# Kernel tuning notes

Hardware: AMD Instinct MI355X
Metric: run time of the kernel (lower is better)

Reference implementation:

```python
import jax, jax.numpy as jnp
import numpy as np

B, S, D, H = 2, 2048, 768, 12
HD = D // H  # head_dim = 64


def setup_inputs() -> dict:
    key = jax.random.key(0)
    ks = jax.random.split(key, 9)
    s = 1.0 / np.sqrt(D)
    return {
        "x": jax.random.normal(ks[0], (B, S, D), dtype=jnp.float32),
        "Wq": jax.random.normal(ks[1], (D, D), dtype=jnp.float32) * s,
        "bq": jnp.zeros((D,), dtype=jnp.float32),
        "Wk": jax.random.normal(ks[2], (D, D), dtype=jnp.float32) * s,
        "bk": jnp.zeros((D,), dtype=jnp.float32),
        "Wv": jax.random.normal(ks[3], (D, D), dtype=jnp.float32) * s,
        "bv": jnp.zeros((D,), dtype=jnp.float32),
        "Wo": jax.random.normal(ks[4], (D, D), dtype=jnp.float32) * s,
        "bo": jnpp if False else jnp.zeros((D,), dtype=jnp.float32),
    }


def reference(x, Wq, bq, Wk, bk, Wv, bv, Wo, bo):
    b, s, d = x.shape
    # projections, split heads: [b, h, s, hd]
    def proj(W, bias):
        y = x @ W + bias
        return y.reshape(b, s, H, HD).transpose(0, 2, 1, 3)

    q = proj(Wq, bq)
    k = proj(Wk, bk)
    v = proj(Wv, bv)

    scale = 1.0 / jnp.sqrt(jnp.float32(HD))
    scores = jnp.einsum("bhqd,bhkd->bhqk", q, k) * scale
    causal = jnp.tril(jnp.ones((s, s), dtype=bool))  # True where allowed
    scores = jnp.where(causal, scores, -jnp.inf)
    attn = jax.nn.softmax(scores, axis=-1)
    ctx = jnp.einsum("bhqk,bhkd->bhqd", attn, v)
    ctx = ctx.transpose(0, 2, 1, 3).reshape(b, s, d)
    return ctx @ Wo + bo
```

## Files before the change

### kernel.cpp

```cpp
#include <hip/hip_runtime.h>
#include <stdint.h>

typedef unsigned short u16;
typedef __attribute__((ext_vector_type(8))) short s16x8;
typedef __attribute__((ext_vector_type(4))) float f32x4;
typedef __attribute__((ext_vector_type(16))) float f32x16;

#define MFMA_BF16(a, b, c) __builtin_amdgcn_mfma_f32_16x16x32_bf16((a), (b), (c), 0, 0, 0)
#define MFMA32(a, b, c) __builtin_amdgcn_mfma_f32_32x32x16_bf16((a), (b), (c), 0, 0, 0)

typedef const __attribute__((address_space(1))) uint32_t* gas1_t;
typedef __attribute__((address_space(3))) uint32_t* las3_t;
#define GLDS16(dst, src) __builtin_amdgcn_global_load_lds((gas1_t)(src), (las3_t)(dst), 16, 0, 0)

static __device__ __forceinline__ u16 f2bf(float f) {
    uint32_t u = __float_as_uint(f);
    u = (u + 0x7fffu + ((u >> 16) & 1u)) >> 16;
    return (u16)u;
}
static __device__ __forceinline__ uint32_t pk2bf(float a, float b) {
    return (uint32_t)f2bf(a) | ((uint32_t)f2bf(b) << 16);
}
static __device__ __forceinline__ float bf2f(u16 h) {
    return __uint_as_float(((uint32_t)h) << 16);
}

__global__ __launch_bounds__(256) void k_prep(const float* __restrict__ x, u16* __restrict__ xb,
                                              const float* __restrict__ w0, const float* __restrict__ w1,
                                              const float* __restrict__ w2, const float* __restrict__ w3,
                                              u16* __restrict__ t0, u16* __restrict__ t1,
                                              u16* __restrict__ t2, u16* __restrict__ t3) {
    __shared__ float tile[32][33];
    const int bid = blockIdx.x, t = threadIdx.x;
    if (bid < 1536) {
        const int i = (bid * 256 + t) * 8;
        f32x4 a = *(const f32x4*)(x + i);
        f32x4 b = *(const f32x4*)(x + i + 4);
        s16x8 r;
        r[0] = (short)f2bf(a[0]); r[1] = (short)f2bf(a[1]);
        r[2] = (short)f2bf(a[2]); r[3] = (short)f2bf(a[3]);
        r[4] = (short)f2bf(b[0]); r[5] = (short)f2bf(b[1]);
        r[6] = (short)f2bf(b[2]); r[7] = (short)f2bf(b[3]);
        *(s16x8*)(xb + i) = r;
        return;
    }
    const int u = bid - 1536;
    const int z = u / 576, r2 = u - z * 576;
    const float* W; u16* T;
    switch (z) {
        case 0:  W = w0; T = t0; break;
        case 1:  W = w1; T = t1; break;
        case 2:  W = w2; T = t2; break;
        default: W = w3; T = t3; break;
    }
    const int n0 = (r2 % 24) * 32, k0 = (r2 / 24) * 32;
    const int tx = t & 31, ty = t >> 5;
#pragma unroll
    for (int i = 0; i < 4; ++i)
        tile[ty + 8 * i][tx] = W[(size_t)(k0 + ty + 8 * i) * 768 + n0 + tx];
    __syncthreads();
#pragma unroll
    for (int i = 0; i < 4; ++i)
        T[(size_t)(n0 + ty + 8 * i) * 768 + k0 + tx] = f2bf(tile[tx][ty + 8 * i]);
}

__global__ __launch_bounds__(256) void k_gemm_qkv(
        const u16* __restrict__ A,
        const u16* __restrict__ btq, const u16* __restrict__ btk, const u16* __restrict__ btv,
        const float* __restrict__ bq, const float* __restrict__ bk, const float* __restrict__ bv,
        u16* __restrict__ outq, u16* __restrict__ outk, u16* __restrict__ outv) {
    __shared__ u16 lA[128 * 64];
    __shared__ u16 lB[64 * 64];
    const int cid = blockIdx.x;
    const int swz = (cid & 7) * 144 + (cid >> 3);
    const int sx = swz % 36, by = swz / 36;
    const int sel = sx / 12, nb = sx - sel * 12;
    const u16* Bt; const float* bias;
    if (sel == 0)      { Bt = btq; bias = bq; }
    else if (sel == 1) { Bt = btk; bias = bk; }
    else               { Bt = btv; bias = bv; }
    const int t = threadIdx.x, lane = t & 63, w = t >> 6;
    const int wr = w >> 1, wc = w & 1;
    const int c = lane & 15, g = lane >> 4;
    const int m0 = by * 128, n0 = nb * 64;
    f32x4 acc[4][2] = {};
    const int lr = lane >> 3, lg = lane & 7;
    const int swz8 = 8 * (lg ^ lr);
    const u16* gA = A  + (size_t)(m0 + w * 8 + lr) * 768 + swz8;
    const u16* gB = Bt + (size_t)(n0 + w * 8 + lr) * 768 + swz8;
    for (int kb = 0; kb < 768; kb += 64) {
#pragma unroll
        for (int j = 0; j < 4; ++j)
            GLDS16(&lA[j * 2048 + w * 512], gA + (size_t)j * 32 * 768 + kb);
#pragma unroll
        for (int j = 0; j < 2; ++j)
            GLDS16(&lB[j * 2048 + w * 512], gB + (size_t)j * 32 * 768 + kb);
        __syncthreads();
#pragma unroll
        for (int kh = 0; kh < 2; ++kh) {
            s16x8 af[4], bfr[2];
            const int gg = kh * 4 + g;
#pragma unroll
            for (int i = 0; i < 4; ++i) {
                const int ra = wr * 64 + i * 16 + c;
                af[i] = *(const s16x8*)&lA[ra * 64 + 8 * (gg ^ (ra & 7))];
            }
#pragma unroll
            for (int j = 0; j < 2; ++j) {
                const int rb = wc * 32 + j * 16 + c;
                bfr[j] = *(const s16x8*)&lB[rb * 64 + 8 * (gg ^ (rb & 7))];
            }
#pragma unroll
            for (int i = 0; i < 4; ++i)
#pragma unroll
                for (int j = 0; j < 2; ++j)
                    acc[i][j] = MFMA_BF16(af[i], bfr[j], acc[i][j]);
        }
        __syncthreads();
    }
    const float C2 = 0.18033688011112042f;
    const int h = nb;
    if (sel < 2) {
        u16* outp = (sel == 0) ? outq : outk;
        const float osc = (sel == 0) ? C2 : 1.0f;
#pragma unroll
        for (int i = 0; i < 4; ++i)
#pragma unroll
            for (int j = 0; j < 2; ++j) {
                const int hd = wc * 32 + j * 16 + c;
                const float bvv = bias[n0 + hd];
#pragma unroll
                for (int rr = 0; rr < 4; ++rr) {
                    const int m = m0 + wr * 64 + i * 16 + g * 4 + rr;
                    const int b = m >> 11, s = m & 2047;
                    outp[(((size_t)(b * 12 + h) * 2048 + s) << 6) + hd] =
                        f2bf((acc[i][j][rr] + bvv) * osc);
                }
            }
    } else {
#pragma unroll
        for (int i = 0; i < 4; ++i)
#pragma unroll
            for (int j = 0; j < 2; ++j) {
                const int hd = wc * 32 + j * 16 + c;
                const float bvv = bias[n0 + hd];
                const int m = m0 + wr * 64 + i * 16 + g * 4;
                const int b = m >> 11, s = m & 2047;
                uint64_t pk = (uint64_t)pk2bf(acc[i][j][0] + bvv, acc[i][j][1] + bvv) |
                              ((uint64_t)pk2bf(acc[i][j][2] + bvv, acc[i][j][3] + bvv) << 32);
                *(uint64_t*)&outv[((size_t)(b * 12 + h) * 64 + hd) * 2048 + s] = pk;
            }
    }
}

__global__ __launch_bounds__(256) void k_gemm_out(const u16* __restrict__ A,
                                                  const u16* __restrict__ Bt,
                                                  const float* __restrict__ bias,
                                                  float* __restrict__ out) {
    __shared__ u16 lA[64 * 64];
    __shared__ u16 lB[64 * 64];
    const int cid = blockIdx.x;
    const int swz = (cid & 7) * 96 + (cid >> 3);
    const int bx = swz % 12, by = swz / 12;
    const int t = threadIdx.x;
    const int lane = t & 63, w = t >> 6;
    const int wr = w >> 1, wc = w & 1;
    const int c = lane & 15, g = lane >> 4;
    const int m0 = by * 64, n0 = bx * 64;
    f32x4 acc[2][2] = {};
    const int lr = lane >> 3, lq = lane & 7;
    const int sq = (lq ^ lr) * 8;
    const u16* gA0 = A  + (size_t)(m0 + w * 16 + lr) * 768 + sq;
    const u16* gA1 = gA0 + 8 * 768;
    const u16* gB0 = Bt + (size_t)(n0 + w * 16 + lr) * 768 + sq;
    const u16* gB1 = gB0 + 8 * 768;
    u16* dA0 = &lA[w * 1024];
    u16* dA1 = &lA[w * 1024 + 512];
    u16* dB0 = &lB[w * 1024];
    u16* dB1 = &lB[w * 1024 + 512];
    for (int kb = 0; kb < 768; kb += 64) {
        GLDS16(dA0, gA0 + kb); GLDS16(dA1, gA1 + kb);
        GLDS16(dB0, gB0 + kb); GLDS16(dB1, gB1 + kb);
        __syncthreads();
#pragma unroll
        for (int st = 0; st < 2; ++st) {
            s16x8 af[2], bf[2];
            const int col = st * 32 + g * 8;
#pragma unroll
            for (int i = 0; i < 2; ++i) {
                int ra = wr * 32 + i * 16 + c;
                af[i] = *(const s16x8*)&lA[ra * 64 + (col ^ ((ra & 7) << 3))];
                int rb = wc * 32 + i * 16 + c;
                bf[i] = *(const s16x8*)&lB[rb * 64 + (col ^ ((rb & 7) << 3))];
            }
#pragma unroll
            for (int i = 0; i < 2; ++i)
#pragma unroll
                for (int j = 0; j < 2; ++j)
                    acc[i][j] = MFMA_BF16(af[i], bf[j], acc[i][j]);
        }
        __syncthreads();
    }
#pragma unroll
    for (int i = 0; i < 2; ++i)
#pragma unroll
        for (int j = 0; j < 2; ++j) {
            const int n = n0 + wc * 32 + j * 16 + c;
            const float bvv = bias[n];
#pragma unroll
            for (int rr = 0; rr < 4; ++rr) {
                const int m = m0 + wr * 32 + i * 16 + g * 4 + rr;
                out[(size_t)m * 768 + n] = acc[i][j][rr] + bvv;
            }
        }
}

__device__ static const signed char SLOT_QT[40] = {
    15,15,15,15, 14,14,14,14, 13,13,13,13, 12,12,12,12,
    11,11,11, 10,10,10, 9,9,9, 8,8,8, 7,7, 6,6, 5,5, 4,4, 3, 2, 1, 0};
__device__ static const signed char SLOT_SEG[40] = {
    0,1,2,3, 0,1,2,3, 0,1,2,3, 0,1,2,3,
    0,1,2, 0,1,2, 0,1,2, 0,1,2, 0,1, 0,1, 0,1, 0,1, 0, 0, 0, 0};

__global__ __launch_bounds__(256) void k_attn(const u16* __restrict__ qw,
                                              const u16* __restrict__ kw,
                                              const u16* __restrict__ vt,
                                              u16* __restrict__ ctxb,
                                              u16* __restrict__ pctx,
                                              float* __restrict__ pm,
                                              float* __restrict__ ps) {
    __shared__ u16 lK[2][64 * 64];
    __shared__ u16 lV[2][64 * 64];
    const int bid = blockIdx.x;
    const int slot = bid / 24, j24 = bid - slot * 24;
    const int bh = (j24 & 7) * 3 + (j24 >> 3);
    const int qt = SLOT_QT[slot], seg = SLOT_SEG[slot];
    const int nseg = (2 * (qt + 1) + 7) >> 3;
    const int ch0 = seg * 8;
    const int rem = 2 * (qt + 1) - ch0;
    const int nch = rem < 8 ? rem : 8;
    const int t = threadIdx.x, lane = t & 63, w = t >> 6;
    const int l31 = lane & 31, hi = lane >> 5;
    const int q0w = qt * 128 + w * 32;
    const u16* qp = qw + (size_t)bh * 2048 * 64;
    const u16* kp = kw + (size_t)bh * 2048 * 64;
    const u16* vp = vt + (size_t)bh * 64 * 2048;
    s16x8 qf[4];
#pragma unroll
    for (int dk = 0; dk < 4; ++dk)
        qf[dk] = *(const s16x8*)&qp[(size_t)(q0w + l31) * 64 + dk * 16 + hi * 8];
    asm volatile("s_waitcnt vmcnt(0)" ::: "memory");
    const int lr = lane >> 3, lg = lane & 7;
    const int swz8 = 8 * (lg ^ lr);
    const u16* kpb = kp + (size_t)(w * 16 + lr) * 64 + swz8;
    const u16* vpb = vp + (size_t)(w * 16 + lr) * 2048 + swz8;
    const int lastq = q0w + 31;
    f32x16 ct[2] = {};
    float m2 = -1e30f, ssum = 0.0f;
#define STAGE(bf, ch)                                                          \
    {                                                                          \
        const u16* ks_ = kpb + (size_t)(ch) * 4096;                            \
        GLDS16(&lK[bf][(w * 16) * 64], ks_);                                   \
        GLDS16(&lK[bf][(w * 16 + 8) * 64], ks_ + 8 * 64);                      \
        const u16* vs_ = vpb + (size_t)(ch) * 64;                              \
        GLDS16(&lV[bf][(w * 16) * 64], vs_);                                   \
        GLDS16(&lV[bf][(w * 16 + 8) * 64], vs_ + 8 * 2048);                    \
    }
    STAGE(0, ch0);
    for (int ci = 0; ci < nch; ++ci) {
        const int bf = ci & 1, Kc = (ch0 + ci) * 64;
        if (ci + 1 < nch) {
            STAGE(bf ^ 1, ch0 + ci + 1);
            asm volatile("s_waitcnt vmcnt(4)" ::: "memory");
        } else {
            asm volatile("s_waitcnt vmcnt(0)" ::: "memory");
        }
        __builtin_amdgcn_sched_barrier(0);
        __builtin_amdgcn_s_barrier();
        if (Kc <= lastq) {
            f32x16 st[2] = {};
            __builtin_amdgcn_s_setprio(1);
#pragma unroll
            for (int dk = 0; dk < 4; ++dk) {
                const int gr = dk * 2 + hi;
                const int r0 = l31, r1 = 32 + l31;
                s16x8 kf0 = *(const s16x8*)&lK[bf][r0 * 64 + 8 * (gr ^ (r0 & 7))];
                s16x8 kf1 = *(const s16x8*)&lK[bf][r1 * 64 + 8 * (gr ^ (r1 & 7))];
                st[0] = MFMA32(kf0, qf[dk], st[0]);
                st[1] = MFMA32(kf1, qf[dk], st[1]);
            }
            __builtin_amdgcn_s_setprio(0);
            const int qg = q0w + l31;
            float tv[32];
            if (Kc + 63 <= q0w) {
#pragma unroll
                for (int j = 0; j < 16; ++j) { tv[j] = st[0][j]; tv[16 + j] = st[1][j]; }
            } else {
                const int kb = Kc + 4 * hi;
#pragma unroll
                for (int j = 0; j < 16; ++j) {
                    const int kloc = (j & 3) + 8 * (j >> 2);
                    tv[j]      = (kb + kloc      <= qg) ? st[0][j] : -1e30f;
                    tv[16 + j] = (kb + kloc + 32 <= qg) ? st[1][j] : -1e30f;
                }
            }
            float x16[16], x8[8], x4[4];
#pragma unroll
            for (int j = 0; j < 16; ++j) x16[j] = fmaxf(tv[j], tv[j + 16]);
#pragma unroll
            for (int j = 0; j < 8; ++j) x8[j] = fmaxf(x16[j], x16[j + 8]);
#pragma unroll
            for (int j = 0; j < 4; ++j) x4[j] = fmaxf(x8[j], x8[j + 4]);
            const float mt = fmaxf(fmaxf(x4[0], x4[1]), fmaxf(x4[2], x4[3]));
            if (!__all(mt <= m2 + 8.0f)) {
                float mq = fmaxf(mt, __shfl_xor(mt, 32));
                const float mnew = fmaxf(m2, mq);
                const float fac = __builtin_amdgcn_exp2f(m2 - mnew);
                ssum *= fac;
#pragma unroll
                for (int j = 0; j < 16; ++j) { ct[0][j] *= fac; ct[1][j] *= fac; }
                m2 = mnew;
            }
            float p[32];
#pragma unroll
            for (int j = 0; j < 32; ++j) p[j] = __builtin_amdgcn_exp2f(tv[j] - m2);
            float y16[16], y8[8], y4[4];
#pragma unroll
            for (int j = 0; j < 16; ++j) y16[j] = p[j] + p[j + 16];
#pragma unroll
            for (int j = 0; j < 8; ++j) y8[j] = y16[j] + y16[j + 8];
#pragma unroll
            for (int j = 0; j < 4; ++j) y4[j] = y8[j] + y8[j + 4];
            ssum += (y4[0] + y4[1]) + (y4[2] + y4[3]);
#pragma unroll
            for (int kt = 0; kt < 2; ++kt) {
                uint32_t pcv[8];
#pragma unroll
                for (int x = 0; x < 8; ++x) {
                    const int j = kt * 16 + 4 * (x >> 1) + 2 * (x & 1);
                    asm volatile("v_cvt_pk_bf16_f32 %0, %1, %2"
                                 : "=v"(pcv[x]) : "v"(p[j]), "v"(p[j + 1]));
                }
#pragma unroll
                for (int kl = 0; kl < 2; ++kl) {
                    uint32_t a0 = pcv[4 * kl],     b0 = pcv[4 * kl + 2];
                    uint32_t a1 = pcv[4 * kl + 1], b1 = pcv[4 * kl + 3];
                    asm volatile("v_permlane32_swap_b32 %0, %1" : "+v"(a0), "+v"(b0));
                    asm volatile("v_permlane32_swap_b32 %0, %1" : "+v"(a1), "+v"(b1));
                    union { uint32_t u[4]; s16x8 v; } pf;
                    pf.u[0] = a0; pf.u[1] = a1; pf.u[2] = b0; pf.u[3] = b1;
                    const int gr = (kt * 2 + kl) * 2 + hi;
                    const int rv0 = l31, rv1 = 32 + l31;
                    s16x8 vf0 = *(const s16x8*)&lV[bf][rv0 * 64 + 8 * (gr ^ (rv0 & 7))];
                    s16x8 vf1 = *(const s16x8*)&lV[bf][rv1 * 64 + 8 * (gr ^ (rv1 & 7))];
                    __builtin_amdgcn_s_setprio(1);
                    ct[0] = MFMA32(vf0, pf.v, ct[0]);
                    ct[1] = MFMA32(vf1, pf.v, ct[1]);
                    __builtin_amdgcn_s_setprio(0);
                }
            }
        }
        __builtin_amdgcn_s_barrier();
    }
    if (nseg == 1) {
        ssum += __shfl_xor(ssum, 32);
        const float inv = 1.0f / ssum;
        const int b = bh / 12, h = bh - b * 12;
        const size_t base = (size_t)(b * 2048 + q0w + l31) * 768 + h * 64;
#pragma unroll
        for (int ht = 0; ht < 2; ++ht)
#pragma unroll
            for (int a = 0; a < 4; ++a) {
                const int hd = ht * 32 + 8 * a + 4 * hi;
                uint64_t pk = (uint64_t)pk2bf(ct[ht][4 * a] * inv, ct[ht][4 * a + 1] * inv) |
                              ((uint64_t)pk2bf(ct[ht][4 * a + 2] * inv, ct[ht][4 * a + 3] * inv) << 32);
                *(uint64_t*)&ctxb[base + hd] = pk;
            }
    } else {
        const float srow = ssum + __shfl_xor(ssum, 32);
        const int ti = (bh * 16 + qt) * 4 + seg;
        const int row = w * 32 + l31;
        u16* pp = &pctx[(size_t)ti * 8192 + row * 64];
#pragma unroll
        for (int ht = 0; ht < 2; ++ht)
#pragma unroll
            for (int a = 0; a < 4; ++a) {
                const int hd = ht * 32 + 8 * a + 4 * hi;
                uint64_t pk = (uint64_t)pk2bf(ct[ht][4 * a], ct[ht][4 * a + 1]) |
                              ((uint64_t)pk2bf(ct[ht][4 * a + 2], ct[ht][4 * a + 3]) << 32);
                *(uint64_t*)&pp[hd] = pk;
            }
        if (hi == 0) {
            pm[ti * 128 + row] = m2;
            ps[ti * 128 + row] = srow;
        }
    }
#undef STAGE
}

__global__ __launch_bounds__(256) void k_attn_combine(const u16* __restrict__ pctx,
                                                      const float* __restrict__ pm,
                                                      const float* __restrict__ ps,
                                                      u16* __restrict__ ctxb) {
    const int bh = blockIdx.x, qt = blockIdx.y + 4;
    const int nseg = (2 * (qt + 1) + 7) >> 3;
    const int tb = (bh * 16 + qt) * 4;
    const int b = bh / 12, h = bh - b * 12;
#pragma unroll
    for (int it = 0; it < 2; ++it) {
        const int u = threadIdx.x + it * 256;
        const int row = u >> 2, h0 = (u & 3) * 16;
        float mv[4], sv[4];
#pragma unroll
        for (int s = 0; s < 4; ++s) {
            mv[s] = (s < nseg) ? pm[(tb + s) * 128 + row] : -1e30f;
            sv[s] = (s < nseg) ? ps[(tb + s) * 128 + row] : 0.0f;
        }
        const float mstar = fmaxf(fmaxf(mv[0], mv[1]), fmaxf(mv[2], mv[3]));
        float wv[4], S = 0.0f;
#pragma unroll
        for (int s = 0; s < 4; ++s) {
            wv[s] = __builtin_amdgcn_exp2f(mv[s] - mstar);
            S += wv[s] * sv[s];
        }
        float acc[16] = {};
#pragma unroll
        for (int s = 0; s < 4; ++s) {
            if (s < nseg) {
                const u16* pp = &pctx[(size_t)(tb + s) * 8192 + row * 64 + h0];
                const float wgt = wv[s];
#pragma unroll
                for (int e = 0; e < 2; ++e) {
                    s16x8 v = *(const s16x8*)(pp + e * 8);
#pragma unroll
                    for (int x = 0; x < 8; ++x)
                        acc[e * 8 + x] += wgt * bf2f((u16)v[x]);
                }
            }
        }
        const float inv = 1.0f / S;
        u16* op = &ctxb[(size_t)(b * 2048 + qt * 128 + row) * 768 + h * 64 + h0];
        s16x8 o0, o1;
#pragma unroll
        for (int x = 0; x < 8; ++x) {
            o0[x] = (short)f2bf(acc[x] * inv);
            o1[x] = (short)f2bf(acc[8 + x] * inv);
        }
        *(s16x8*)op = o0;
        *(s16x8*)(op + 8) = o1;
    }
}

extern "C" void kernel_launch(void* const* d_in, const int* in_sizes, int n_in,
                              void* d_out, int out_size, void* d_ws, size_t ws_size,
                              hipStream_t stream) {
    (void)in_sizes; (void)n_in; (void)out_size; (void)ws_size;
    const float* x  = (const float*)d_in[0];
    const float* Wq = (const float*)d_in[1];
    const float* bq = (const float*)d_in[2];
    const float* Wk = (const float*)d_in[3];
    const float* bk = (const float*)d_in[4];
    const float* Wv = (const float*)d_in[5];
    const float* bv = (const float*)d_in[6];
    const float* Wo = (const float*)d_in[7];
    const float* bo = (const float*)d_in[8];
    char* ws = (char*)d_ws;
    u16* xb   = (u16*)(ws);
    u16* wqt  = (u16*)(ws + 6291456);
    u16* wkt  = (u16*)(ws + 7471104);
    u16* wvt  = (u16*)(ws + 8650752);
    u16* wot  = (u16*)(ws + 9830400);
    u16* qwv  = (u16*)(ws + 11010048);
    u16* kwv  = (u16*)(ws + 17301504);
    u16* vtw  = (u16*)(ws + 23592960);
    u16* ctx  = (u16*)(ws + 29884416);
    u16* pctx = (u16*)(ws + 36175872);
    float* pm = (float*)(ws + 61341696);
    float* psu= (float*)(ws + 62128128);
    float* out = (float*)d_out;

    k_prep<<<3840, 256, 0, stream>>>(x, xb, Wq, Wk, Wv, Wo, wqt, wkt, wvt, wot);
    k_gemm_qkv<<<1152, 256, 0, stream>>>(xb, wqt, wkt, wvt, bq, bk, bv, qwv, kwv, vtw);
    k_attn<<<960, 256, 0, stream>>>(qwv, kwv, vtw, ctx, pctx, pm, psu);
    k_attn_combine<<<dim3(24, 12), 256, 0, stream>>>(pctx, pm, psu, ctx);
    k_gemm_out<<<768, 256, 0, stream>>>(ctx, wot, bo, out);
}
```

Measured before the change: 160.6 us.

## Double-buffer GEMM LDS tiles and read attention K/V straight from global

Both projection GEMMs now double-buffer their LDS tiles. The next K-slice is issued with global_load_lds before computing on the current one, using vmcnt waits and a single barrier per iteration. The attention kernel drops its LDS staging of K and V entirely: each wave loads its K rows and V columns directly from global memory and skips chunks beyond its last causal query, with no block barriers. This aims to overlap load latency with MFMA work in the GEMMs and to remove barrier stalls in attention. The cost is doubled LDS in the GEMMs and redundant, possibly less coalesced, global and L2 traffic for K and V in attention.

```diff
diff --git a/kernel.cpp b/kernel.cpp
--- a/kernel.cpp
+++ b/kernel.cpp
@@ -69,8 +69,8 @@
         const u16* __restrict__ btq, const u16* __restrict__ btk, const u16* __restrict__ btv,
         const float* __restrict__ bq, const float* __restrict__ bk, const float* __restrict__ bv,
         u16* __restrict__ outq, u16* __restrict__ outk, u16* __restrict__ outv) {
-    __shared__ u16 lA[128 * 64];
-    __shared__ u16 lB[64 * 64];
+    __shared__ u16 lA[2][128 * 64];
+    __shared__ u16 lB[2][64 * 64];
     const int cid = blockIdx.x;
     const int swz = (cid & 7) * 144 + (cid >> 3);
     const int sx = swz % 36, by = swz / 36;
@@ -88,14 +88,26 @@
     const int swz8 = 8 * (lg ^ lr);
     const u16* gA = A  + (size_t)(m0 + w * 8 + lr) * 768 + swz8;
     const u16* gB = Bt + (size_t)(n0 + w * 8 + lr) * 768 + swz8;
-    for (int kb = 0; kb < 768; kb += 64) {
-#pragma unroll
-        for (int j = 0; j < 4; ++j)
-            GLDS16(&lA[j * 2048 + w * 512], gA + (size_t)j * 32 * 768 + kb);
-#pragma unroll
-        for (int j = 0; j < 2; ++j)
-            GLDS16(&lB[j * 2048 + w * 512], gB + (size_t)j * 32 * 768 + kb);
-        __syncthreads();
+#define STG_QKV(bb, kb)                                                        \
+    {                                                                          \
+        _Pragma("unroll")                                                      \
+        for (int j = 0; j < 4; ++j)                                            \
+            GLDS16(&lA[bb][j * 2048 + w * 512], gA + (size_t)j * 32 * 768 + (kb)); \
+        _Pragma("unroll")                                                      \
+        for (int j = 0; j < 2; ++j)                                            \
+            GLDS16(&lB[bb][j * 2048 + w * 512], gB + (size_t)j * 32 * 768 + (kb)); \
+    }
+    STG_QKV(0, 0);
+    for (int ki = 0; ki < 12; ++ki) {
+        const int cur = ki & 1;
+        if (ki + 1 < 12) {
+            STG_QKV(cur ^ 1, (ki + 1) * 64);
+            asm volatile("s_waitcnt vmcnt(6)" ::: "memory");
+        } else {
+            asm volatile("s_waitcnt vmcnt(0)" ::: "memory");
+        }
+        __builtin_amdgcn_sched_barrier(0);
+        __builtin_amdgcn_s_barrier();
 #pragma unroll
         for (int kh = 0; kh < 2; ++kh) {
             s16x8 af[4], bfr[2];
@@ -103,12 +115,12 @@
 #pragma unroll
             for (int i = 0; i < 4; ++i) {
                 const int ra = wr * 64 + i * 16 + c;
-                af[i] = *(const s16x8*)&lA[ra * 64 + 8 * (gg ^ (ra & 7))];
+                af[i] = *(const s16x8*)&lA[cur][ra * 64 + 8 * (gg ^ (ra & 7))];
             }
 #pragma unroll
             for (int j = 0; j < 2; ++j) {
                 const int rb = wc * 32 + j * 16 + c;
-                bfr[j] = *(const s16x8*)&lB[rb * 64 + 8 * (gg ^ (rb & 7))];
+                bfr[j] = *(const s16x8*)&lB[cur][rb * 64 + 8 * (gg ^ (rb & 7))];
             }
 #pragma unroll
             for (int i = 0; i < 4; ++i)
@@ -116,8 +128,9 @@
                 for (int j = 0; j < 2; ++j)
                     acc[i][j] = MFMA_BF16(af[i], bfr[j], acc[i][j]);
         }
-        __syncthreads();
-    }
+        __builtin_amdgcn_s_barrier();
+    }
+#undef STG_QKV
     const float C2 = 0.18033688011112042f;
     const int h = nb;
     if (sel < 2) {
@@ -157,8 +170,8 @@
                                                   const u16* __restrict__ Bt,
                                                   const float* __restrict__ bias,
                                                   float* __restrict__ out) {
-    __shared__ u16 lA[64 * 64];
-    __shared__ u16 lB[64 * 64];
+    __shared__ u16 lA[2][64 * 64];
+    __shared__ u16 lB[2][64 * 64];
     const int cid = blockIdx.x;
     const int swz = (cid & 7) * 96 + (cid >> 3);
     const int bx = swz % 12, by = swz / 12;
@@ -174,14 +187,24 @@
     const u16* gA1 = gA0 + 8 * 768;
     const u16* gB0 = Bt + (size_t)(n0 + w * 16 + lr) * 768 + sq;
     const u16* gB1 = gB0 + 8 * 768;
-    u16* dA0 = &lA[w * 1024];
-    u16* dA1 = &lA[w * 1024 + 512];
-    u16* dB0 = &lB[w * 1024];
-    u16* dB1 = &lB[w * 1024 + 512];
-    for (int kb = 0; kb < 768; kb += 64) {
-        GLDS16(dA0, gA0 + kb); GLDS16(dA1, gA1 + kb);
-        GLDS16(dB0, gB0 + kb); GLDS16(dB1, gB1 + kb);
-        __syncthreads();
+#define STG_OUT(bb, kb)                                                        \
+    {                                                                          \
+        GLDS16(&lA[bb][w * 1024], gA0 + (kb));                                 \
+        GLDS16(&lA[bb][w * 1024 + 512], gA1 + (kb));                           \
+        GLDS16(&lB[bb][w * 1024], gB0 + (kb));                                 \
+        GLDS16(&lB[bb][w * 1024 + 512], gB1 + (kb));                           \
+    }
+    STG_OUT(0, 0);
+    for (int ki = 0; ki < 12; ++ki) {
+        const int cur = ki & 1;
+        if (ki + 1 < 12) {
+            STG_OUT(cur ^ 1, (ki + 1) * 64);
+            asm volatile("s_waitcnt vmcnt(4)" ::: "memory");
+        } else {
+            asm volatile("s_waitcnt vmcnt(0)" ::: "memory");
+        }
+        __builtin_amdgcn_sched_barrier(0);
+        __builtin_amdgcn_s_barrier();
 #pragma unroll
         for (int st = 0; st < 2; ++st) {
             s16x8 af[2], bf[2];
@@ -189,9 +212,9 @@
 #pragma unroll
             for (int i = 0; i < 2; ++i) {
                 int ra = wr * 32 + i * 16 + c;
-                af[i] = *(const s16x8*)&lA[ra * 64 + (col ^ ((ra & 7) << 3))];
+                af[i] = *(const s16x8*)&lA[cur][ra * 64 + (col ^ ((ra & 7) << 3))];
                 int rb = wc * 32 + i * 16 + c;
-                bf[i] = *(const s16x8*)&lB[rb * 64 + (col ^ ((rb & 7) << 3))];
+                bf[i] = *(const s16x8*)&lB[cur][rb * 64 + (col ^ ((rb & 7) << 3))];
             }
 #pragma unroll
             for (int i = 0; i < 2; ++i)
@@ -199,8 +222,9 @@
                 for (int j = 0; j < 2; ++j)
                     acc[i][j] = MFMA_BF16(af[i], bf[j], acc[i][j]);
         }
-        __syncthreads();
-    }
+        __builtin_amdgcn_s_barrier();
+    }
+#undef STG_OUT
 #pragma unroll
     for (int i = 0; i < 2; ++i)
 #pragma unroll
@@ -229,8 +253,6 @@
                                               u16* __restrict__ pctx,
                                               float* __restrict__ pm,
                                               float* __restrict__ ps) {
-    __shared__ u16 lK[2][64 * 64];
-    __shared__ u16 lV[2][64 * 64];
     const int bid = blockIdx.x;
     const int slot = bid / 24, j24 = bid - slot * 24;
     const int bh = (j24 & 7) * 3 + (j24 >> 3);
@@ -249,118 +271,90 @@
 #pragma unroll
     for (int dk = 0; dk < 4; ++dk)
         qf[dk] = *(const s16x8*)&qp[(size_t)(q0w + l31) * 64 + dk * 16 + hi * 8];
-    asm volatile("s_waitcnt vmcnt(0)" ::: "memory");
-    const int lr = lane >> 3, lg = lane & 7;
-    const int swz8 = 8 * (lg ^ lr);
-    const u16* kpb = kp + (size_t)(w * 16 + lr) * 64 + swz8;
-    const u16* vpb = vp + (size_t)(w * 16 + lr) * 2048 + swz8;
     const int lastq = q0w + 31;
+    const int lastch = (lastq >> 6) + 1 - ch0;
+    const int mynch = nch < lastch ? nch : lastch;
     f32x16 ct[2] = {};
     float m2 = -1e30f, ssum = 0.0f;
-#define STAGE(bf, ch)                                                          \
-    {                                                                          \
-        const u16* ks_ = kpb + (size_t)(ch) * 4096;                            \
-        GLDS16(&lK[bf][(w * 16) * 64], ks_);                                   \
-        GLDS16(&lK[bf][(w * 16 + 8) * 64], ks_ + 8 * 64);                      \
-        const u16* vs_ = vpb + (size_t)(ch) * 64;                              \
-        GLDS16(&lV[bf][(w * 16) * 64], vs_);                                   \
-        GLDS16(&lV[bf][(w * 16 + 8) * 64], vs_ + 8 * 2048);                    \
-    }
-    STAGE(0, ch0);
-    for (int ci = 0; ci < nch; ++ci) {
-        const int bf = ci & 1, Kc = (ch0 + ci) * 64;
-        if (ci + 1 < nch) {
-            STAGE(bf ^ 1, ch0 + ci + 1);
-            asm volatile("s_waitcnt vmcnt(4)" ::: "memory");
+    for (int ci = 0; ci < mynch; ++ci) {
+        const int Kc = (ch0 + ci) * 64;
+        const u16* kr0 = kp + (size_t)(Kc + l31) * 64;
+        const u16* kr1 = kp + (size_t)(Kc + 32 + l31) * 64;
+        f32x16 st[2] = {};
+#pragma unroll
+        for (int dk = 0; dk < 4; ++dk) {
+            const int gr = dk * 2 + hi;
+            s16x8 kf0 = *(const s16x8*)&kr0[gr * 8];
+            s16x8 kf1 = *(const s16x8*)&kr1[gr * 8];
+            st[0] = MFMA32(kf0, qf[dk], st[0]);
+            st[1] = MFMA32(kf1, qf[dk], st[1]);
+        }
+        const int qg = q0w + l31;
+        float tv[32];
+        if (Kc + 63 <= q0w) {
+#pragma unroll
+            for (int j = 0; j < 16; ++j) { tv[j] = st[0][j]; tv[16 + j] = st[1][j]; }
         } else {
-            asm volatile("s_waitcnt vmcnt(0)" ::: "memory");
-        }
-        __builtin_amdgcn_sched_barrier(0);
-        __builtin_amdgcn_s_barrier();
-        if (Kc <= lastq) {
-            f32x16 st[2] = {};
-            __builtin_amdgcn_s_setprio(1);
-#pragma unroll
-            for (int dk = 0; dk < 4; ++dk) {
-                const int gr = dk * 2 + hi;
-                const int r0 = l31, r1 = 32 + l31;
-                s16x8 kf0 = *(const s16x8*)&lK[bf][r0 * 64 + 8 * (gr ^ (r0 & 7))];
-                s16x8 kf1 = *(const s16x8*)&lK[bf][r1 * 64 + 8 * (gr ^ (r1 & 7))];
-                st[0] = MFMA32(kf0, qf[dk], st[0]);
-                st[1] = MFMA32(kf1, qf[dk], st[1]);
-            }
-            __builtin_amdgcn_s_setprio(0);
-            const int qg = q0w + l31;
-            float tv[32];
-            if (Kc + 63 <= q0w) {
-#pragma unroll
-                for (int j = 0; j < 16; ++j) { tv[j] = st[0][j]; tv[16 + j] = st[1][j]; }
-            } else {
-                const int kb = Kc + 4 * hi;
-#pragma unroll
-                for (int j = 0; j < 16; ++j) {
-                    const int kloc = (j & 3) + 8 * (j >> 2);
-                    tv[j]      = (kb + kloc      <= qg) ? st[0][j] : -1e30f;
-                    tv[16 + j] = (kb + kloc + 32 <= qg) ? st[1][j] : -1e30f;
-                }
-            }
-            float x16[16], x8[8], x4[4];
-#pragma unroll
-            for (int j = 0; j < 16; ++j) x16[j] = fmaxf(tv[j], tv[j + 16]);
-#pragma unroll
-            for (int j = 0; j < 8; ++j) x8[j] = fmaxf(x16[j], x16[j + 8]);
-#pragma unroll
-            for (int j = 0; j < 4; ++j) x4[j] = fmaxf(x8[j], x8[j + 4]);
-            const float mt = fmaxf(fmaxf(x4[0], x4[1]), fmaxf(x4[2], x4[3]));
-            if (!__all(mt <= m2 + 8.0f)) {
-                float mq = fmaxf(mt, __shfl_xor(mt, 32));
-                const float mnew = fmaxf(m2, mq);
-                const float fac = __builtin_amdgcn_exp2f(m2 - mnew);
-                ssum *= fac;
-#pragma unroll
-                for (int j = 0; j < 16; ++j) { ct[0][j] *= fac; ct[1][j] *= fac; }
-                m2 = mnew;
-            }
-            float p[32];
-#pragma unroll
-            for (int j = 0; j < 32; ++j) p[j] = __builtin_amdgcn_exp2f(tv[j] - m2);
-            float y16[16], y8[8], y4[4];
-#pragma unroll
-            for (int j = 0; j < 16; ++j) y16[j] = p[j] + p[j + 16];
-#pragma unroll
-            for (int j = 0; j < 8; ++j) y8[j] = y16[j] + y16[j + 8];
-#pragma unroll
-            for (int j = 0; j < 4; ++j) y4[j] = y8[j] + y8[j + 4];
-            ssum += (y4[0] + y4[1]) + (y4[2] + y4[3]);
-#pragma unroll
-            for (int kt = 0; kt < 2; ++kt) {
-                uint32_t pcv[8];
-#pragma unroll
-                for (int x = 0; x < 8; ++x) {
-                    const int j = kt * 16 + 4 * (x >> 1) + 2 * (x & 1);
-                    asm volatile("v_cvt_pk_bf16_f32 %0, %1, %2"
-                                 : "=v"(pcv[x]) : "v"(p[j]), "v"(p[j + 1]));
-                }
-#pragma unroll
-                for (int kl = 0; kl < 2; ++kl) {
-                    uint32_t a0 = pcv[4 * kl],     b0 = pcv[4 * kl + 2];
-                    uint32_t a1 = pcv[4 * kl + 1], b1 = pcv[4 * kl + 3];
-                    asm volatile("v_permlane32_swap_b32 %0, %1" : "+v"(a0), "+v"(b0));
-                    asm volatile("v_permlane32_swap_b32 %0, %1" : "+v"(a1), "+v"(b1));
-                    union { uint32_t u[4]; s16x8 v; } pf;
-                    pf.u[0] = a0; pf.u[1] = a1; pf.u[2] = b0; pf.u[3] = b1;
-                    const int gr = (kt * 2 + kl) * 2 + hi;
-                    const int rv0 = l31, rv1 = 32 + l31;
-                    s16x8 vf0 = *(const s16x8*)&lV[bf][rv0 * 64 + 8 * (gr ^ (rv0 & 7))];
-                    s16x8 vf1 = *(const s16x8*)&lV[bf][rv1 * 64 + 8 * (gr ^ (rv1 & 7))];
-                    __builtin_amdgcn_s_setprio(1);
-                    ct[0] = MFMA32(vf0, pf.v, ct[0]);
-                    ct[1] = MFMA32(vf1, pf.v, ct[1]);
-                    __builtin_amdgcn_s_setprio(0);
-                }
-            }
-        }
-        __builtin_amdgcn_s_barrier();
+            const int kb = Kc + 4 * hi;
+#pragma unroll
+            for (int j = 0; j < 16; ++j) {
+                const int kloc = (j & 3) + 8 * (j >> 2);
+                tv[j]      = (kb + kloc      <= qg) ? st[0][j] : -1e30f;
+                tv[16 + j] = (kb + kloc + 32 <= qg) ? st[1][j] : -1e30f;
+            }
+        }
+        float x16[16], x8[8], x4[4];
+#pragma unroll
+        for (int j = 0; j < 16; ++j) x16[j] = fmaxf(tv[j], tv[j + 16]);
+#pragma unroll
+        for (int j = 0; j < 8; ++j) x8[j] = fmaxf(x16[j], x16[j + 8]);
+#pragma unroll
+        for (int j = 0; j < 4; ++j) x4[j] = fmaxf(x8[j], x8[j + 4]);
+        const float mt = fmaxf(fmaxf(x4[0], x4[1]), fmaxf(x4[2], x4[3]));
+        if (!__all(mt <= m2 + 8.0f)) {
+            float mq = fmaxf(mt, __shfl_xor(mt, 32));
+            const float mnew = fmaxf(m2, mq);
+            const float fac = __builtin_amdgcn_exp2f(m2 - mnew);
+            ssum *= fac;
+#pragma unroll
+            for (int j = 0; j < 16; ++j) { ct[0][j] *= fac; ct[1][j] *= fac; }
+            m2 = mnew;
+        }
+        float p[32];
+#pragma unroll
+        for (int j = 0; j < 32; ++j) p[j] = __builtin_amdgcn_exp2f(tv[j] - m2);
+        float y16[16], y8[8], y4[4];
+#pragma unroll
+        for (int j = 0; j < 16; ++j) y16[j] = p[j] + p[j + 16];
+#pragma unroll
+        for (int j = 0; j < 8; ++j) y8[j] = y16[j] + y16[j + 8];
+#pragma unroll
+        for (int j = 0; j < 4; ++j) y4[j] = y8[j] + y8[j + 4];
+        ssum += (y4[0] + y4[1]) + (y4[2] + y4[3]);
+#pragma unroll
+        for (int kt = 0; kt < 2; ++kt) {
+            uint32_t pcv[8];
+#pragma unroll
+            for (int x = 0; x < 8; ++x) {
+                const int j = kt * 16 + 4 * (x >> 1) + 2 * (x & 1);
+                asm volatile("v_cvt_pk_bf16_f32 %0, %1, %2"
+                             : "=v"(pcv[x]) : "v"(p[j]), "v"(p[j + 1]));
+            }
+#pragma unroll
+            for (int kl = 0; kl < 2; ++kl) {
+                uint32_t a0 = pcv[4 * kl],     b0 = pcv[4 * kl + 2];
+                uint32_t a1 = pcv[4 * kl + 1], b1 = pcv[4 * kl + 3];
+                asm volatile("v_permlane32_swap_b32 %0, %1" : "+v"(a0), "+v"(b0));
+                asm volatile("v_permlane32_swap_b32 %0, %1" : "+v"(a1), "+v"(b1));
+                union { uint32_t u[4]; s16x8 v; } pf;
+                pf.u[0] = a0; pf.u[1] = a1; pf.u[2] = b0; pf.u[3] = b1;
+                const int ko = Kc + (kt * 2 + kl) * 16 + hi * 8;
+                s16x8 vf0 = *(const s16x8*)&vp[(size_t)l31 * 2048 + ko];
+                s16x8 vf1 = *(const s16x8*)&vp[(size_t)(32 + l31) * 2048 + ko];
+                ct[0] = MFMA32(vf0, pf.v, ct[0]);
+                ct[1] = MFMA32(vf1, pf.v, ct[1]);
+            }
+        }
     }
     if (nseg == 1) {
         ssum += __shfl_xor(ssum, 32);
@@ -395,7 +389,6 @@
             ps[ti * 128 + row] = srow;
         }
     }
-#undef STAGE
 }
 
 __global__ __launch_bounds__(256) void k_attn_combine(const u16* __restrict__ pctx,
```

Measured after the change: 187.7 us. 16.9% more time.
